# Kernel tuning notes

Hardware: AMD Instinct MI355X
Metric: run time of the kernel (lower is better)

The kernel has to match this reference:

```python
import jax, jax.numpy as jnp
import numpy as np

N = 8192
D = 200


def setup_inputs() -> dict:
    key = jax.random.key(0)
    k1, k2, k3 = jax.random.split(key, 3)
    G_p = jax.random.normal(k1, (N, D), dtype=jnp.float32)
    # scale weights so exp(b + e) stays in a sane numeric range
    wb = jax.random.normal(k2, (D, 1), dtype=jnp.float32) * 0.02
    we = jax.random.normal(k3, (D, 1), dtype=jnp.float32) * 0.02
    return {"G_p": G_p, "wb": wb, "we": we, "k": 100}


def reference(G_p, wb, we, k):
    # begin / end scores: [N, 1]
    b_P = G_p @ wb
    e_P = G_p @ we
    # outer-sum span scores -> [N, N]
    numerator = jnp.exp(b_P + e_P.T)
    denominator = jnp.sum(numerator)
    candidate_probs = numerator / denominator
    upper = jnp.triu(candidate_probs)
    flat = upper.reshape(-1)
    k_max_values, flat_idx = jax.lax.top_k(flat, k)
    W = upper.shape[1]
    orig_indices = jnp.stack([flat_idx // W, flat_idx % W], axis=1)
    return orig_indices, k_max_values
```

## Files before the change

kernel.cpp:

```cpp
#include <hip/hip_runtime.h>
#include <math.h>

#define NN 8192
#define DD 200
#define KK 100

#define NBINS 1024
#define HSCALE 64.0f
#define BINW 0.015625f
#define CAND_CAP 4096
#define ROW_CAP 1024

#define OFF_B 0
#define OFF_E 8192

__global__ __launch_bounds__(256) void k_be(const float* __restrict__ G,
                                            const float* __restrict__ wb,
                                            const float* __restrict__ we,
                                            float* __restrict__ wsf) {
    int gid = blockIdx.x * 256 + threadIdx.x;
    int row = gid >> 6;
    int lane = gid & 63;
    float pb = 0.f, pe = 0.f;
    if (lane < 50) {
        float4 g = ((const float4*)(G + (size_t)row * DD))[lane];
        float4 B = ((const float4*)wb)[lane];
        float4 E = ((const float4*)we)[lane];
        pb = fmaf(g.x, B.x, fmaf(g.y, B.y, fmaf(g.z, B.z, g.w * B.w)));
        pe = fmaf(g.x, E.x, fmaf(g.y, E.y, fmaf(g.z, E.z, g.w * E.w)));
    }
    for (int off = 32; off; off >>= 1) {
        pb += __shfl_xor(pb, off, 64);
        pe += __shfl_xor(pe, off, 64);
    }
    if (lane == 0) { wsf[OFF_B + row] = pb; wsf[OFF_E + row] = pe; }
}

__global__ __launch_bounds__(1024) void k_tail(const float* __restrict__ wsf,
                                               float* __restrict__ out) {
    __shared__ float    b_s[NN];
    __shared__ float    e_s[NN];
    __shared__ float    cv[CAND_CAP];
    __shared__ unsigned ci[CAND_CAP];
    __shared__ unsigned sfx[NBINS];
    __shared__ unsigned hbl[NBINS];
    __shared__ int      rows_s[ROW_CAP];
    __shared__ float    rowb_s[ROW_CAP];
    __shared__ float    fred[1024];
    __shared__ unsigned wred[16];
    __shared__ unsigned cnt_s, nrows_s, ncand_s;

    int tid = threadIdx.x, wave = tid >> 6, lane = tid & 63;

    sfx[tid] = 0u; hbl[tid] = 0u;
    if (tid == 0) { nrows_s = 0u; ncand_s = 0u; }
    __syncthreads();
    float leb = 0.f, lee = 0.f, lem = -1e30f;
    for (int i = tid; i < NN; i += 1024) {
        float bv = wsf[OFF_B + i], ev = wsf[OFF_E + i];
        b_s[i] = bv; e_s[i] = ev;
        leb += expf(bv); lee += expf(ev); lem = fmaxf(lem, ev);
        int p = (int)fmaf(bv, HSCALE, 512.f); p = min(max(p, 0), NBINS - 1);
        int q = (int)fmaf(ev, HSCALE, 512.f); q = min(max(q, 0), NBINS - 1);
        atomicAdd(&hbl[p], 1u);
        atomicAdd(&sfx[q], 1u);
    }
    fred[tid] = leb; __syncthreads();
    for (int off = 512; off; off >>= 1) { if (tid < off) fred[tid] += fred[tid + off]; __syncthreads(); }
    float sb = fred[0]; __syncthreads();
    fred[tid] = lee; __syncthreads();
    for (int off = 512; off; off >>= 1) { if (tid < off) fred[tid] += fred[tid + off]; __syncthreads(); }
    float se = fred[0]; __syncthreads();
    fred[tid] = lem; __syncthreads();
    for (int off = 512; off; off >>= 1) { if (tid < off) fred[tid] = fmaxf(fred[tid], fred[tid + off]); __syncthreads(); }
    float emax = fred[0]; __syncthreads();

    for (int d = 1; d < NBINS; d <<= 1) {
        unsigned v = (tid + d < NBINS) ? sfx[tid + d] : 0u;
        __syncthreads();
        sfx[tid] += v;
        __syncthreads();
    }
    int lo = 0, hi = NBINS - 1;
    while (lo < hi) {
        int mid = (lo + hi + 1) >> 1;
        int idx = mid + 512 - tid;
        unsigned sv = (idx <= 0) ? sfx[0] : ((idx > NBINS - 1) ? 0u : sfx[idx]);
        unsigned c = hbl[tid] * sv;
        for (int off = 32; off; off >>= 1) c += __shfl_xor(c, off, 64);
        if (lane == 0) wred[wave] = c;
        __syncthreads();
        if (tid == 0) {
            unsigned tot = 0;
            for (int i = 0; i < 16; ++i) tot += wred[i];
            cnt_s = tot;
        }
        __syncthreads();
        if (cnt_s >= 2 * KK) lo = mid; else hi = mid - 1;
        __syncthreads();
    }
    float thr = -8.0f + (float)(lo - 1) * BINW;

    for (int i = tid; i < NN; i += 1024) {
        float bi = b_s[i];
        if (bi + emax >= thr) {
            unsigned pos = atomicAdd(&nrows_s, 1u);
            if (pos < ROW_CAP) { rows_s[pos] = i; rowb_s[pos] = bi; }
        }
    }
    __syncthreads();

    int nr = min(nrows_s, (unsigned)ROW_CAP);
    for (int ri = 0; ri < nr; ++ri) {
        int r = rows_s[ri];
        float bi = rowb_s[ri];
        for (int j = r + tid; j < NN; j += 1024) {
            float s = bi + e_s[j];
            if (s >= thr) {
                unsigned pos = atomicAdd(&ncand_s, 1u);
                if (pos < CAND_CAP) {
                    cv[pos] = s;
                    ci[pos] = ((unsigned)r << 13) | (unsigned)j;
                }
            }
        }
    }
    __syncthreads();

    unsigned M = min(ncand_s, (unsigned)CAND_CAP);
    float inv_den = 1.0f / (sb * se);
    for (unsigned c = tid; c < M; c += 1024) {
        float v = cv[c];
        unsigned fi = ci[c];
        int rank = 0;
        for (unsigned m = 0; m < M; ++m) {
            float vm = cv[m];
            rank += (vm > v) || (vm == v && ci[m] < fi);
        }
        if (rank < KK) {
            out[2 * rank]     = (float)(fi >> 13);
            out[2 * rank + 1] = (float)(fi & 8191u);
            out[200 + rank]   = expf(v) * inv_den;
        }
    }
}

extern "C" void kernel_launch(void* const* d_in, const int* in_sizes, int n_in,
                              void* d_out, int out_size, void* d_ws, size_t ws_size,
                              hipStream_t stream) {
    const float* G  = (const float*)d_in[0];
    const float* wb = (const float*)d_in[1];
    const float* we = (const float*)d_in[2];
    float* out = (float*)d_out;
    float* wsf = (float*)d_ws;

    hipLaunchKernelGGL(k_be, dim3(2048), dim3(256), 0, stream, G, wb, we, wsf);
    hipLaunchKernelGGL(k_tail, dim3(1), dim3(1024), 0, stream, wsf, out);
}
```

Before: 93.54 us.

## Cut barriers in tail kernel and prune candidate columns as well as rows

Replaces the tree reductions in shared memory with wave shuffle reductions, does the suffix scan with in-wave shuffles plus a per-wave tail offset, and swaps the 10-step binary search for a 3-round radix-16 search that evaluates 16 thresholds in parallel. Candidate generation now prunes columns by bmax as well as rows by emax, and enumerates only the row×column cross product instead of scanning full rows serially. This cuts many __syncthreads and serial row loops in the single-block tail kernel. The trade-off is capped column lists (COL_CAP), which could drop candidates if too many columns pass.

```diff
diff --git a/kernel.cpp b/kernel.cpp
--- a/kernel.cpp
+++ b/kernel.cpp
@@ -10,6 +10,7 @@
 #define BINW 0.015625f
 #define CAND_CAP 4096
 #define ROW_CAP 1024
+#define COL_CAP 1024
 
 #define OFF_B 0
 #define OFF_E 8192
@@ -46,101 +47,154 @@
     __shared__ unsigned hbl[NBINS];
     __shared__ int      rows_s[ROW_CAP];
     __shared__ float    rowb_s[ROW_CAP];
-    __shared__ float    fred[1024];
-    __shared__ unsigned wred[16];
-    __shared__ unsigned cnt_s, nrows_s, ncand_s;
+    __shared__ int      cols_s[COL_CAP];
+    __shared__ float    cole_s[COL_CAP];
+    __shared__ float    fr_sb[16], fr_se[16], fr_em[16], fr_bm[16];
+    __shared__ unsigned wred[16], wtail_s[16];
+    __shared__ unsigned nrows_s, ncols_s, ncand_s;
+    __shared__ int      lo_s;
+    __shared__ float    sums_s[4];
 
     int tid = threadIdx.x, wave = tid >> 6, lane = tid & 63;
 
     sfx[tid] = 0u; hbl[tid] = 0u;
-    if (tid == 0) { nrows_s = 0u; ncand_s = 0u; }
-    __syncthreads();
-    float leb = 0.f, lee = 0.f, lem = -1e30f;
+    if (tid == 0) { nrows_s = 0u; ncols_s = 0u; ncand_s = 0u; lo_s = 0; }
+    __syncthreads();
+
+    float leb = 0.f, lee = 0.f, lem = -1e30f, lbm = -1e30f;
     for (int i = tid; i < NN; i += 1024) {
         float bv = wsf[OFF_B + i], ev = wsf[OFF_E + i];
         b_s[i] = bv; e_s[i] = ev;
-        leb += expf(bv); lee += expf(ev); lem = fmaxf(lem, ev);
+        leb += expf(bv); lee += expf(ev);
+        lem = fmaxf(lem, ev); lbm = fmaxf(lbm, bv);
         int p = (int)fmaf(bv, HSCALE, 512.f); p = min(max(p, 0), NBINS - 1);
         int q = (int)fmaf(ev, HSCALE, 512.f); q = min(max(q, 0), NBINS - 1);
         atomicAdd(&hbl[p], 1u);
         atomicAdd(&sfx[q], 1u);
     }
-    fred[tid] = leb; __syncthreads();
-    for (int off = 512; off; off >>= 1) { if (tid < off) fred[tid] += fred[tid + off]; __syncthreads(); }
-    float sb = fred[0]; __syncthreads();
-    fred[tid] = lee; __syncthreads();
-    for (int off = 512; off; off >>= 1) { if (tid < off) fred[tid] += fred[tid + off]; __syncthreads(); }
-    float se = fred[0]; __syncthreads();
-    fred[tid] = lem; __syncthreads();
-    for (int off = 512; off; off >>= 1) { if (tid < off) fred[tid] = fmaxf(fred[tid], fred[tid + off]); __syncthreads(); }
-    float emax = fred[0]; __syncthreads();
-
-    for (int d = 1; d < NBINS; d <<= 1) {
-        unsigned v = (tid + d < NBINS) ? sfx[tid + d] : 0u;
-        __syncthreads();
-        sfx[tid] += v;
-        __syncthreads();
-    }
-    int lo = 0, hi = NBINS - 1;
-    while (lo < hi) {
-        int mid = (lo + hi + 1) >> 1;
-        int idx = mid + 512 - tid;
-        unsigned sv = (idx <= 0) ? sfx[0] : ((idx > NBINS - 1) ? 0u : sfx[idx]);
-        unsigned c = hbl[tid] * sv;
+    for (int off = 32; off; off >>= 1) {
+        leb += __shfl_xor(leb, off, 64);
+        lee += __shfl_xor(lee, off, 64);
+        lem = fmaxf(lem, __shfl_xor(lem, off, 64));
+        lbm = fmaxf(lbm, __shfl_xor(lbm, off, 64));
+    }
+    if (lane == 0) { fr_sb[wave] = leb; fr_se[wave] = lee; fr_em[wave] = lem; fr_bm[wave] = lbm; }
+    __syncthreads();
+    if (tid == 0) {
+        float a = 0.f, b = 0.f, c = -1e30f, d = -1e30f;
+        for (int i = 0; i < 16; ++i) {
+            a += fr_sb[i]; b += fr_se[i];
+            c = fmaxf(c, fr_em[i]); d = fmaxf(d, fr_bm[i]);
+        }
+        sums_s[0] = a; sums_s[1] = b; sums_s[2] = c; sums_s[3] = d;
+    }
+
+    unsigned v = sfx[tid];
+    for (int off = 1; off < 64; off <<= 1) {
+        unsigned t = __shfl_down(v, off, 64);
+        if (lane + off < 64) v += t;
+    }
+    if (lane == 0) wtail_s[wave] = v;
+    __syncthreads();
+    if (tid == 0) {
+        unsigned acc = 0, tails[16];
+        for (int w = 15; w >= 0; --w) { tails[w] = acc; acc += wtail_s[w]; }
+        for (int w = 0; w < 16; ++w) wtail_s[w] = tails[w];
+    }
+    __syncthreads();
+    sfx[tid] = v + wtail_s[wave];
+    __syncthreads();
+
+    const unsigned TARGET = 2u * KK;
+    int chunk = 64;
+    for (int round = 0; round < 2; ++round) {
+        int t = lo_s + (wave + 1) * chunk;
+        unsigned c = 0;
+        for (int k = 0; k < 16; ++k) {
+            int p = lane + (k << 6);
+            int idx = t + 512 - p;
+            unsigned sv = (idx <= 0) ? sfx[0] : ((idx > NBINS - 1) ? 0u : sfx[idx]);
+            c += hbl[p] * sv;
+        }
         for (int off = 32; off; off >>= 1) c += __shfl_xor(c, off, 64);
         if (lane == 0) wred[wave] = c;
         __syncthreads();
         if (tid == 0) {
-            unsigned tot = 0;
-            for (int i = 0; i < 16; ++i) tot += wred[i];
-            cnt_s = tot;
-        }
-        __syncthreads();
-        if (cnt_s >= 2 * KK) lo = mid; else hi = mid - 1;
-        __syncthreads();
-    }
-    float thr = -8.0f + (float)(lo - 1) * BINW;
+            for (int w = 15; w >= 0; --w)
+                if (wred[w] >= TARGET) { lo_s += (w + 1) * chunk; break; }
+        }
+        __syncthreads();
+        chunk >>= 4;
+    }
+    {
+        int t = lo_s + wave + 1;
+        if (wave < 3) {
+            unsigned c = 0;
+            for (int k = 0; k < 16; ++k) {
+                int p = lane + (k << 6);
+                int idx = t + 512 - p;
+                unsigned sv = (idx <= 0) ? sfx[0] : ((idx > NBINS - 1) ? 0u : sfx[idx]);
+                c += hbl[p] * sv;
+            }
+            for (int off = 32; off; off >>= 1) c += __shfl_xor(c, off, 64);
+            if (lane == 0) wred[wave] = c;
+        }
+        __syncthreads();
+        if (tid == 0) {
+            for (int w = 2; w >= 0; --w)
+                if (wred[w] >= TARGET) { lo_s += w + 1; break; }
+        }
+        __syncthreads();
+    }
+    float thr = -8.0f + (float)(lo_s - 1) * BINW;
+    float emax = sums_s[2], bmax = sums_s[3];
 
     for (int i = tid; i < NN; i += 1024) {
-        float bi = b_s[i];
-        if (bi + emax >= thr) {
+        float bv = b_s[i];
+        if (bv + emax >= thr) {
             unsigned pos = atomicAdd(&nrows_s, 1u);
-            if (pos < ROW_CAP) { rows_s[pos] = i; rowb_s[pos] = bi; }
-        }
-    }
-    __syncthreads();
-
-    int nr = min(nrows_s, (unsigned)ROW_CAP);
-    for (int ri = 0; ri < nr; ++ri) {
-        int r = rows_s[ri];
-        float bi = rowb_s[ri];
-        for (int j = r + tid; j < NN; j += 1024) {
-            float s = bi + e_s[j];
-            if (s >= thr) {
-                unsigned pos = atomicAdd(&ncand_s, 1u);
-                if (pos < CAND_CAP) {
-                    cv[pos] = s;
-                    ci[pos] = ((unsigned)r << 13) | (unsigned)j;
-                }
+            if (pos < ROW_CAP) { rows_s[pos] = i; rowb_s[pos] = bv; }
+        }
+        float ev = e_s[i];
+        if (ev + bmax >= thr) {
+            unsigned pos = atomicAdd(&ncols_s, 1u);
+            if (pos < COL_CAP) { cols_s[pos] = i; cole_s[pos] = ev; }
+        }
+    }
+    __syncthreads();
+    int nr = (int)min(nrows_s, (unsigned)ROW_CAP);
+    int nc = (int)min(ncols_s, (unsigned)COL_CAP);
+
+    int tot = nr * nc;
+    for (int idx = tid; idx < tot; idx += 1024) {
+        int ri = idx / nc, cj = idx - ri * nc;
+        int r = rows_s[ri], j = cols_s[cj];
+        if (j < r) continue;
+        float s = rowb_s[ri] + cole_s[cj];
+        if (s >= thr) {
+            unsigned pos = atomicAdd(&ncand_s, 1u);
+            if (pos < CAND_CAP) {
+                cv[pos] = s;
+                ci[pos] = ((unsigned)r << 13) | (unsigned)j;
             }
         }
     }
     __syncthreads();
 
     unsigned M = min(ncand_s, (unsigned)CAND_CAP);
-    float inv_den = 1.0f / (sb * se);
-    for (unsigned c = tid; c < M; c += 1024) {
-        float v = cv[c];
-        unsigned fi = ci[c];
+    float inv_den = 1.0f / (sums_s[0] * sums_s[1]);
+    for (unsigned c2 = tid; c2 < M; c2 += 1024) {
+        float vv = cv[c2];
+        unsigned fi = ci[c2];
         int rank = 0;
         for (unsigned m = 0; m < M; ++m) {
             float vm = cv[m];
-            rank += (vm > v) || (vm == v && ci[m] < fi);
+            rank += (vm > vv) || (vm == vv && ci[m] < fi);
         }
         if (rank < KK) {
             out[2 * rank]     = (float)(fi >> 13);
             out[2 * rank + 1] = (float)(fi & 8191u);
-            out[200 + rank]   = expf(v) * inv_den;
+            out[200 + rank]   = expf(vv) * inv_den;
         }
     }
 }
```

Measured after the change: 80.13 us. 14.3% less time.
